# Performance work log

Hardware: AMD Instinct MI355X
Metric: run time of the kernel (lower is better)

Reference implementation:

```python
import jax, jax.numpy as jnp
import numpy as np

N_NODES = 100000
N_EDGES = 3200000
D_IN = 512
D_HID = 512
D_OUT = 256


def setup_inputs() -> dict:
    key = jax.random.key(0)
    ks = jax.random.split(key, 7)
    x = jax.random.normal(ks[0], (N_NODES, D_IN), dtype=jnp.float32)
    edge_row = jax.random.randint(ks[1], (N_EDGES,), 0, N_NODES, dtype=jnp.int32)
    edge_col = jax.random.randint(ks[2], (N_EDGES,), 0, N_NODES, dtype=jnp.int32)
    edge_val = jax.random.uniform(ks[3], (N_EDGES,), dtype=jnp.float32)
    # Kaiming-uniform-ish init like torch Linear (bias=False)
    W0 = jax.random.normal(ks[4], (D_HID, D_IN), dtype=jnp.float32) / np.sqrt(D_IN)
    W1 = jax.random.normal(ks[5], (D_HID, D_HID), dtype=jnp.float32) / np.sqrt(D_HID)
    W2 = jax.random.normal(ks[6], (D_OUT, D_HID), dtype=jnp.float32) / np.sqrt(D_HID)
    return {"x": x, "edge_row": edge_row, "edge_col": edge_col,
            "edge_val": edge_val, "W0": W0, "W1": W1, "W2": W2}


def reference(x, edge_row, edge_col, edge_val, W0, W1, W2):
    # Layer 0: Linear (no bias) then sparse adjacency matmul (COO segment-sum)
    h = jnp.einsum('nd,hd->nh', x, W0)                      # [N, D_HID]
    msgs = edge_val[:, None] * h[edge_col]                  # gather source features [E, D_HID]
    h = jax.ops.segment_sum(msgs, edge_row, num_segments=N_NODES)  # scatter-add to rows
    h = jax.nn.relu(h)                                      # dropout p=0.0 -> identity
    # Middle layer (num_hidden=3 -> one middle layer): Linear + ReLU
    h = jax.nn.relu(jnp.einsum('nd,hd->nh', h, W1))
    # Final layer: Linear only
    out = jnp.einsum('nd,od->no', h, W2)                    # [N, D_OUT]
    return out
```

## Files before the change

### kernel.cpp

```cpp
#include <hip/hip_runtime.h>

typedef short  s16x8 __attribute__((ext_vector_type(8)));
typedef __bf16 bf16x8 __attribute__((ext_vector_type(8)));
typedef float  f32x4 __attribute__((ext_vector_type(4)));

#define AS1(p) ((const __attribute__((address_space(1))) void*)(p))
#define AS3(p) ((__attribute__((address_space(3))) void*)(p))

__device__ __forceinline__ float bf2f(short x){
  unsigned u = ((unsigned)(unsigned short)x) << 16;
  return __builtin_bit_cast(float, u);
}

__global__ void cast_f32_bf16(const float* __restrict__ in, __bf16* __restrict__ out, int n8){
  int stride = gridDim.x * blockDim.x;
  for (int i = blockIdx.x * blockDim.x + threadIdx.x; i < n8; i += stride){
    const float4* p = (const float4*)in + 2*(size_t)i;
    float4 a = p[0], b = p[1];
    bf16x8 o;
    o[0]=(__bf16)a.x; o[1]=(__bf16)a.y; o[2]=(__bf16)a.z; o[3]=(__bf16)a.w;
    o[4]=(__bf16)b.x; o[5]=(__bf16)b.y; o[6]=(__bf16)b.z; o[7]=(__bf16)b.w;
    ((bf16x8*)out)[i] = o;
  }
}

__global__ void hist_rows(const int* __restrict__ rows, int* __restrict__ counts, int n){
  int stride = gridDim.x * blockDim.x;
  for (int i = blockIdx.x * blockDim.x + threadIdx.x; i < n; i += stride)
    atomicAdd(&counts[rows[i]], 1);
}

__global__ __launch_bounds__(256) void scan_phaseA(const int* __restrict__ counts,
    int* __restrict__ rp, int* __restrict__ bsum, int n4){
  __shared__ int sb[256];
  int t = threadIdx.x;
  int idx = blockIdx.x * 256 + t;
  int4 c = make_int4(0,0,0,0);
  if (idx < n4) c = ((const int4*)counts)[idx];
  int s = c.x + c.y + c.z + c.w;
  sb[t] = s; __syncthreads();
  #pragma unroll
  for (int d = 1; d < 256; d <<= 1){
    int v = (t >= d) ? sb[t - d] : 0;
    __syncthreads();
    sb[t] += v;
    __syncthreads();
  }
  int ex = sb[t] - s;
  if (idx < n4){
    int4 o; o.x = ex; o.y = ex + c.x; o.z = o.y + c.y; o.w = o.z + c.z;
    ((int4*)rp)[idx] = o;
  }
  if (t == 255) bsum[blockIdx.x] = sb[255];
}

__global__ __launch_bounds__(128) void scan_phaseB(int* __restrict__ bsum, int nb){
  __shared__ int sb[128];
  int t = threadIdx.x;
  int v = (t < nb) ? bsum[t] : 0;
  sb[t] = v; __syncthreads();
  #pragma unroll
  for (int d = 1; d < 128; d <<= 1){
    int u = (t >= d) ? sb[t - d] : 0;
    __syncthreads();
    sb[t] += u;
    __syncthreads();
  }
  if (t < nb) bsum[t] = sb[t] - v;
}

__global__ void scan_phaseC(const int* __restrict__ bsum, int* __restrict__ rp,
    int* __restrict__ cursor, int n, int ne){
  int i = blockIdx.x * 256 + threadIdx.x;
  if (i < n){
    int v = rp[i] + bsum[i >> 10];
    rp[i] = v; cursor[i] = v;
  }
  if (i == 0) rp[n] = ne;
}

__global__ void scatter_edges(const int* __restrict__ rows, const int* __restrict__ cols,
    const float* __restrict__ vals, int* __restrict__ cursor,
    int2* __restrict__ ev, int n){
  int stride = gridDim.x * blockDim.x;
  for (int i = blockIdx.x * blockDim.x + threadIdx.x; i < n; i += stride){
    int r = rows[i];
    int p = atomicAdd(&cursor[r], 1);
    ev[p] = make_int2(cols[i], __float_as_int(vals[i]));
  }
}

__global__ __launch_bounds__(256) void spmm_relu(
    const int* __restrict__ rp, const int2* __restrict__ ev,
    const __bf16* __restrict__ H, __bf16* __restrict__ O, int n){
  int w = (blockIdx.x * 256 + threadIdx.x) >> 6;
  int lane = threadIdx.x & 63;
  if (w >= n) return;
  int s = rp[w], e = rp[w + 1];
  int deg = e - s;
  const __bf16* Hl = H + lane * 8;
  float acc[8] = {0,0,0,0,0,0,0,0};

  int2 cv = make_int2(0, 0);
  if (lane < deg) cv = ev[s + lane];
  int m = deg < 64 ? deg : 64;
  int i = 0;
  for (; i + 4 <= m; i += 4){
    int c0 = __builtin_amdgcn_readlane(cv.x, i);
    int c1 = __builtin_amdgcn_readlane(cv.x, i + 1);
    int c2 = __builtin_amdgcn_readlane(cv.x, i + 2);
    int c3 = __builtin_amdgcn_readlane(cv.x, i + 3);
    float v0 = __builtin_bit_cast(float, __builtin_amdgcn_readlane(cv.y, i));
    float v1 = __builtin_bit_cast(float, __builtin_amdgcn_readlane(cv.y, i + 1));
    float v2 = __builtin_bit_cast(float, __builtin_amdgcn_readlane(cv.y, i + 2));
    float v3 = __builtin_bit_cast(float, __builtin_amdgcn_readlane(cv.y, i + 3));
    s16x8 h0 = *(const s16x8*)(Hl + (size_t)c0 * 512);
    s16x8 h1 = *(const s16x8*)(Hl + (size_t)c1 * 512);
    s16x8 h2 = *(const s16x8*)(Hl + (size_t)c2 * 512);
    s16x8 h3 = *(const s16x8*)(Hl + (size_t)c3 * 512);
    #pragma unroll
    for (int k = 0; k < 8; k++){
      acc[k] = fmaf(v0, bf2f(h0[k]), acc[k]);
      acc[k] = fmaf(v1, bf2f(h1[k]), acc[k]);
      acc[k] = fmaf(v2, bf2f(h2[k]), acc[k]);
      acc[k] = fmaf(v3, bf2f(h3[k]), acc[k]);
    }
  }
  for (; i < m; i++){
    int c = __builtin_amdgcn_readlane(cv.x, i);
    float v = __builtin_bit_cast(float, __builtin_amdgcn_readlane(cv.y, i));
    s16x8 h0 = *(const s16x8*)(Hl + (size_t)c * 512);
    #pragma unroll
    for (int k = 0; k < 8; k++) acc[k] = fmaf(v, bf2f(h0[k]), acc[k]);
  }
  for (int j = s + 64; j < e; j++){
    int2 p = ev[j];
    float v = __builtin_bit_cast(float, p.y);
    s16x8 h0 = *(const s16x8*)(Hl + (size_t)p.x * 512);
    #pragma unroll
    for (int k = 0; k < 8; k++) acc[k] = fmaf(v, bf2f(h0[k]), acc[k]);
  }

  s16x8 o;
  #pragma unroll
  for (int k = 0; k < 8; k++){
    float v = fmaxf(acc[k], 0.f);
    o[k] = __builtin_bit_cast(short, (__bf16)v);
  }
  *(s16x8*)(O + (size_t)w * 512 + lane * 8) = o;
}

template<int RELU, int OUT_BF16>
__global__ __launch_bounds__(256) void gemm_bt(
    const __bf16* __restrict__ A, const __bf16* __restrict__ B,
    void* __restrict__ C, int M, int N, int K){
  __shared__ __attribute__((aligned(16))) __bf16 As[128 * 64];
  __shared__ __attribute__((aligned(16))) __bf16 Bs[128 * 64];
  const int ntiles = N >> 7;
  const int tm = blockIdx.x / ntiles;
  const int tn = blockIdx.x % ntiles;
  const int row0 = tm << 7, col0 = tn << 7;
  const int tid = threadIdx.x;
  const int lane = tid & 63, wid = tid >> 6;
  const int wm = (wid >> 1) * 64, wn = (wid & 1) * 64;
  const int lr = lane & 15;
  const int lkb = ((lane >> 4) * 8) * 2;

  f32x4 acc[4][4] = {};

  for (int k0 = 0; k0 < K; k0 += 64){
    __syncthreads();
    #pragma unroll
    for (int i = 0; i < 4; i++){
      int bo = tid * 16 + i * 4096;
      int r  = bo >> 7;
      int cb = bo & 127;
      int ga = row0 + r; ga = ga < M ? ga : M - 1;
      __builtin_amdgcn_global_load_lds(AS1(A + (size_t)ga * K + k0 + (cb >> 1)),
                                       AS3((char*)As + (wid << 10) + i * 4096), 16, 0, 0);
      int gb = col0 + r;
      __builtin_amdgcn_global_load_lds(AS1(B + (size_t)gb * K + k0 + (cb >> 1)),
                                       AS3((char*)Bs + (wid << 10) + i * 4096), 16, 0, 0);
    }
    __syncthreads();
    #pragma unroll
    for (int kk = 0; kk < 2; kk++){
      s16x8 af[4], bfr[4];
      #pragma unroll
      for (int i = 0; i < 4; i++)
        af[i] = *(const s16x8*)((const char*)As + (wm + i * 16 + lr) * 128 + kk * 64 + lkb);
      #pragma unroll
      for (int j = 0; j < 4; j++)
        bfr[j] = *(const s16x8*)((const char*)Bs + (wn + j * 16 + lr) * 128 + kk * 64 + lkb);
      #pragma unroll
      for (int i = 0; i < 4; i++)
        #pragma unroll
        for (int j = 0; j < 4; j++)
          acc[i][j] = __builtin_amdgcn_mfma_f32_16x16x32_bf16(af[i], bfr[j], acc[i][j], 0, 0, 0);
    }
  }

  const int orow = (lane >> 4) * 4;
  #pragma unroll
  for (int i = 0; i < 4; i++){
    #pragma unroll
    for (int j = 0; j < 4; j++){
      int gc = col0 + wn + j * 16 + lr;
      #pragma unroll
      for (int r = 0; r < 4; r++){
        int gr = row0 + wm + i * 16 + orow + r;
        if (gr < M){
          float v = acc[i][j][r];
          if (RELU) v = fmaxf(v, 0.f);
          if (OUT_BF16) ((__bf16*)C)[(size_t)gr * N + gc] = (__bf16)v;
          else          ((float*)C)[(size_t)gr * N + gc] = v;
        }
      }
    }
  }
}

extern "C" void kernel_launch(void* const* d_in, const int* in_sizes, int n_in,
                              void* d_out, int out_size, void* d_ws, size_t ws_size,
                              hipStream_t stream){
  const float* x    = (const float*)d_in[0];
  const int*   erow = (const int*)d_in[1];
  const int*   ecol = (const int*)d_in[2];
  const float* eval = (const float*)d_in[3];
  const float* W0   = (const float*)d_in[4];
  const float* W1   = (const float*)d_in[5];
  const float* W2   = (const float*)d_in[6];

  const int DIN = 512, DH = 512, DO = 256;
  const int NN = in_sizes[0] / DIN;
  const int NE = in_sizes[1];

  size_t off = 0;
  auto carve = [&](size_t b) -> char* {
    char* p = (char*)d_ws + off; off += (b + 255) & ~(size_t)255; return p;
  };
  __bf16* bufA  = (__bf16*)carve((size_t)NN * DIN * 2);
  __bf16* bufB  = (__bf16*)carve((size_t)NN * DH * 2);
  __bf16* wW0   = (__bf16*)carve((size_t)DH * DIN * 2);
  __bf16* wW1   = (__bf16*)carve((size_t)DH * DH * 2);
  __bf16* wW2   = (__bf16*)carve((size_t)DO * DH * 2);
  int*   counts = (int*)carve((size_t)NN * 4);
  int*   rp     = (int*)carve(((size_t)NN + 1) * 4);
  int*   cursor = (int*)carve((size_t)NN * 4);
  int*   bsum   = (int*)carve(4096);
  int2*  ev     = (int2*)carve((size_t)NE * 8);

  hipMemsetAsync(counts, 0, (size_t)NN * 4, stream);

  cast_f32_bf16<<<4096, 256, 0, stream>>>(x,  bufA, NN * DIN / 8);
  cast_f32_bf16<<<256,  256, 0, stream>>>(W0, wW0, DH * DIN / 8);
  cast_f32_bf16<<<256,  256, 0, stream>>>(W1, wW1, DH * DH / 8);
  cast_f32_bf16<<<128,  256, 0, stream>>>(W2, wW2, DO * DH / 8);

  hist_rows<<<2048, 256, 0, stream>>>(erow, counts, NE);
  const int n4 = NN / 4;
  const int nblkA = (n4 + 255) / 256;
  scan_phaseA<<<nblkA, 256, 0, stream>>>(counts, rp, bsum, n4);
  scan_phaseB<<<1, 128, 0, stream>>>(bsum, nblkA);
  scan_phaseC<<<(NN + 255) / 256, 256, 0, stream>>>(bsum, rp, cursor, NN, NE);
  scatter_edges<<<2048, 256, 0, stream>>>(erow, ecol, eval, cursor, ev, NE);

  const int mt = (NN + 127) / 128;
  gemm_bt<0,1><<<dim3(mt * (DH / 128)), 256, 0, stream>>>(bufA, wW0, bufB, NN, DH, DIN);
  spmm_relu<<<(NN * 64 + 255) / 256, 256, 0, stream>>>(rp, ev, bufB, bufA, NN);
  gemm_bt<1,1><<<dim3(mt * (DH / 128)), 256, 0, stream>>>(bufA, wW1, bufB, NN, DH, DH);
  gemm_bt<0,0><<<dim3(mt * (DO / 128)), 256, 0, stream>>>(bufB, wW2, d_out, NN, DO, DH);
}
```

Measured before the change: 1.450 ms.

## Persistent SpMM waves with next-row prefetch, XCD-aware GEMM tile remap, fuse weight casts

The SpMM kernel becomes persistent: 2048 blocks' waves loop over rows with a stride and prefetch the next row's pointers and edge list while the current row is being computed. This hides the latency of the row-pointer and edge loads and cuts wave launch overhead. The GEMM remaps block indices so consecutive tiles land on the same XCD, which should improve L2 reuse of the A row panels. The three weight cast launches are merged into one kernel to save launch overhead. The risk is that the fixed grid may load-balance poorly across rows of different degree.

```diff
diff --git a/kernel.cpp b/kernel.cpp
--- a/kernel.cpp
+++ b/kernel.cpp
@@ -21,6 +21,25 @@
     o[0]=(__bf16)a.x; o[1]=(__bf16)a.y; o[2]=(__bf16)a.z; o[3]=(__bf16)a.w;
     o[4]=(__bf16)b.x; o[5]=(__bf16)b.y; o[6]=(__bf16)b.z; o[7]=(__bf16)b.w;
     ((bf16x8*)out)[i] = o;
+  }
+}
+
+__global__ void cast3_f32_bf16(const float* __restrict__ a, __bf16* __restrict__ oa, int na8,
+                               const float* __restrict__ b, __bf16* __restrict__ ob, int nb8,
+                               const float* __restrict__ c, __bf16* __restrict__ oc, int nc8){
+  int stride = gridDim.x * blockDim.x;
+  int tot = na8 + nb8 + nc8;
+  for (int i = blockIdx.x * blockDim.x + threadIdx.x; i < tot; i += stride){
+    const float* in; __bf16* out; int j = i;
+    if (j < na8){ in = a; out = oa; }
+    else if (j < na8 + nb8){ j -= na8; in = b; out = ob; }
+    else { j -= na8 + nb8; in = c; out = oc; }
+    const float4* p = (const float4*)in + 2*(size_t)j;
+    float4 u = p[0], v = p[1];
+    bf16x8 o;
+    o[0]=(__bf16)u.x; o[1]=(__bf16)u.y; o[2]=(__bf16)u.z; o[3]=(__bf16)u.w;
+    o[4]=(__bf16)v.x; o[5]=(__bf16)v.y; o[6]=(__bf16)v.z; o[7]=(__bf16)v.w;
+    ((bf16x8*)out)[j] = o;
   }
 }
 
@@ -92,62 +111,76 @@
 
 __global__ __launch_bounds__(256) void spmm_relu(
     const int* __restrict__ rp, const int2* __restrict__ ev,
-    const __bf16* __restrict__ H, __bf16* __restrict__ O, int n){
+    const __bf16* __restrict__ H, __bf16* __restrict__ O, int n, int nwaves){
+  int lane = threadIdx.x & 63;
   int w = (blockIdx.x * 256 + threadIdx.x) >> 6;
-  int lane = threadIdx.x & 63;
   if (w >= n) return;
+  const __bf16* Hl = H + lane * 8;
+
   int s = rp[w], e = rp[w + 1];
-  int deg = e - s;
-  const __bf16* Hl = H + lane * 8;
-  float acc[8] = {0,0,0,0,0,0,0,0};
-
   int2 cv = make_int2(0, 0);
-  if (lane < deg) cv = ev[s + lane];
-  int m = deg < 64 ? deg : 64;
-  int i = 0;
-  for (; i + 4 <= m; i += 4){
-    int c0 = __builtin_amdgcn_readlane(cv.x, i);
-    int c1 = __builtin_amdgcn_readlane(cv.x, i + 1);
-    int c2 = __builtin_amdgcn_readlane(cv.x, i + 2);
-    int c3 = __builtin_amdgcn_readlane(cv.x, i + 3);
-    float v0 = __builtin_bit_cast(float, __builtin_amdgcn_readlane(cv.y, i));
-    float v1 = __builtin_bit_cast(float, __builtin_amdgcn_readlane(cv.y, i + 1));
-    float v2 = __builtin_bit_cast(float, __builtin_amdgcn_readlane(cv.y, i + 2));
-    float v3 = __builtin_bit_cast(float, __builtin_amdgcn_readlane(cv.y, i + 3));
-    s16x8 h0 = *(const s16x8*)(Hl + (size_t)c0 * 512);
-    s16x8 h1 = *(const s16x8*)(Hl + (size_t)c1 * 512);
-    s16x8 h2 = *(const s16x8*)(Hl + (size_t)c2 * 512);
-    s16x8 h3 = *(const s16x8*)(Hl + (size_t)c3 * 512);
+  if (lane < e - s) cv = ev[s + lane];
+
+  while (true){
+    int wn = w + nwaves;
+    int sn = 0, en = 0;
+    int2 cvn = make_int2(0, 0);
+    if (wn < n){
+      sn = rp[wn]; en = rp[wn + 1];
+      if (lane < en - sn) cvn = ev[sn + lane];
+    }
+
+    float acc[8] = {0,0,0,0,0,0,0,0};
+    int deg = e - s;
+    int m = deg < 64 ? deg : 64;
+    int i = 0;
+    for (; i + 4 <= m; i += 4){
+      int c0 = __builtin_amdgcn_readlane(cv.x, i);
+      int c1 = __builtin_amdgcn_readlane(cv.x, i + 1);
+      int c2 = __builtin_amdgcn_readlane(cv.x, i + 2);
+      int c3 = __builtin_amdgcn_readlane(cv.x, i + 3);
+      float v0 = __builtin_bit_cast(float, __builtin_amdgcn_readlane(cv.y, i));
+      float v1 = __builtin_bit_cast(float, __builtin_amdgcn_readlane(cv.y, i + 1));
+      float v2 = __builtin_bit_cast(float, __builtin_amdgcn_readlane(cv.y, i + 2));
+      float v3 = __builtin_bit_cast(float, __builtin_amdgcn_readlane(cv.y, i + 3));
+      s16x8 h0 = *(const s16x8*)(Hl + (size_t)c0 * 512);
+      s16x8 h1 = *(const s16x8*)(Hl + (size_t)c1 * 512);
+      s16x8 h2 = *(const s16x8*)(Hl + (size_t)c2 * 512);
+      s16x8 h3 = *(const s16x8*)(Hl + (size_t)c3 * 512);
+      #pragma unroll
+      for (int k = 0; k < 8; k++){
+        acc[k] = fmaf(v0, bf2f(h0[k]), acc[k]);
+        acc[k] = fmaf(v1, bf2f(h1[k]), acc[k]);
+        acc[k] = fmaf(v2, bf2f(h2[k]), acc[k]);
+        acc[k] = fmaf(v3, bf2f(h3[k]), acc[k]);
+      }
+    }
+    for (; i < m; i++){
+      int c = __builtin_amdgcn_readlane(cv.x, i);
+      float v = __builtin_bit_cast(float, __builtin_amdgcn_readlane(cv.y, i));
+      s16x8 h0 = *(const s16x8*)(Hl + (size_t)c * 512);
+      #pragma unroll
+      for (int k = 0; k < 8; k++) acc[k] = fmaf(v, bf2f(h0[k]), acc[k]);
+    }
+    for (int j = s + 64; j < e; j++){
+      int2 p = ev[j];
+      float v = __builtin_bit_cast(float, p.y);
+      s16x8 h0 = *(const s16x8*)(Hl + (size_t)p.x * 512);
+      #pragma unroll
+      for (int k = 0; k < 8; k++) acc[k] = fmaf(v, bf2f(h0[k]), acc[k]);
+    }
+
+    s16x8 o;
     #pragma unroll
     for (int k = 0; k < 8; k++){
-      acc[k] = fmaf(v0, bf2f(h0[k]), acc[k]);
-      acc[k] = fmaf(v1, bf2f(h1[k]), acc[k]);
-      acc[k] = fmaf(v2, bf2f(h2[k]), acc[k]);
-      acc[k] = fmaf(v3, bf2f(h3[k]), acc[k]);
-    }
-  }
-  for (; i < m; i++){
-    int c = __builtin_amdgcn_readlane(cv.x, i);
-    float v = __builtin_bit_cast(float, __builtin_amdgcn_readlane(cv.y, i));
-    s16x8 h0 = *(const s16x8*)(Hl + (size_t)c * 512);
-    #pragma unroll
-    for (int k = 0; k < 8; k++) acc[k] = fmaf(v, bf2f(h0[k]), acc[k]);
-  }
-  for (int j = s + 64; j < e; j++){
-    int2 p = ev[j];
-    float v = __builtin_bit_cast(float, p.y);
-    s16x8 h0 = *(const s16x8*)(Hl + (size_t)p.x * 512);
-    #pragma unroll
-    for (int k = 0; k < 8; k++) acc[k] = fmaf(v, bf2f(h0[k]), acc[k]);
-  }
-
-  s16x8 o;
-  #pragma unroll
-  for (int k = 0; k < 8; k++){
-    float v = fmaxf(acc[k], 0.f);
-    o[k] = __builtin_bit_cast(short, (__bf16)v);
-  }
-  *(s16x8*)(O + (size_t)w * 512 + lane * 8) = o;
+      float v = fmaxf(acc[k], 0.f);
+      o[k] = __builtin_bit_cast(short, (__bf16)v);
+    }
+    *(s16x8*)(O + (size_t)w * 512 + lane * 8) = o;
+
+    if (wn >= n) break;
+    w = wn; s = sn; e = en; cv = cvn;
+  }
 }
 
 template<int RELU, int OUT_BF16>
@@ -156,9 +189,13 @@
     void* __restrict__ C, int M, int N, int K){
   __shared__ __attribute__((aligned(16))) __bf16 As[128 * 64];
   __shared__ __attribute__((aligned(16))) __bf16 Bs[128 * 64];
+  const int nwg = gridDim.x;
+  const int q = nwg >> 3, r = nwg & 7;
+  const int xcd = blockIdx.x & 7, idx = blockIdx.x >> 3;
+  const int wg = (xcd < r ? xcd * (q + 1) : r * (q + 1) + (xcd - r) * q) + idx;
   const int ntiles = N >> 7;
-  const int tm = blockIdx.x / ntiles;
-  const int tn = blockIdx.x % ntiles;
+  const int tm = wg / ntiles;
+  const int tn = wg % ntiles;
   const int row0 = tm << 7, col0 = tn << 7;
   const int tid = threadIdx.x;
   const int lane = tid & 63, wid = tid >> 6;
@@ -173,12 +210,12 @@
     #pragma unroll
     for (int i = 0; i < 4; i++){
       int bo = tid * 16 + i * 4096;
-      int r  = bo >> 7;
+      int rr = bo >> 7;
       int cb = bo & 127;
-      int ga = row0 + r; ga = ga < M ? ga : M - 1;
+      int ga = row0 + rr; ga = ga < M ? ga : M - 1;
       __builtin_amdgcn_global_load_lds(AS1(A + (size_t)ga * K + k0 + (cb >> 1)),
                                        AS3((char*)As + (wid << 10) + i * 4096), 16, 0, 0);
-      int gb = col0 + r;
+      int gb = col0 + rr;
       __builtin_amdgcn_global_load_lds(AS1(B + (size_t)gb * K + k0 + (cb >> 1)),
                                        AS3((char*)Bs + (wid << 10) + i * 4096), 16, 0, 0);
     }
@@ -207,10 +244,10 @@
     for (int j = 0; j < 4; j++){
       int gc = col0 + wn + j * 16 + lr;
       #pragma unroll
-      for (int r = 0; r < 4; r++){
-        int gr = row0 + wm + i * 16 + orow + r;
+      for (int rr = 0; rr < 4; rr++){
+        int gr = row0 + wm + i * 16 + orow + rr;
         if (gr < M){
-          float v = acc[i][j][r];
+          float v = acc[i][j][rr];
           if (RELU) v = fmaxf(v, 0.f);
           if (OUT_BF16) ((__bf16*)C)[(size_t)gr * N + gc] = (__bf16)v;
           else          ((float*)C)[(size_t)gr * N + gc] = v;
@@ -252,10 +289,10 @@
 
   hipMemsetAsync(counts, 0, (size_t)NN * 4, stream);
 
-  cast_f32_bf16<<<4096, 256, 0, stream>>>(x,  bufA, NN * DIN / 8);
-  cast_f32_bf16<<<256,  256, 0, stream>>>(W0, wW0, DH * DIN / 8);
-  cast_f32_bf16<<<256,  256, 0, stream>>>(W1, wW1, DH * DH / 8);
-  cast_f32_bf16<<<128,  256, 0, stream>>>(W2, wW2, DO * DH / 8);
+  cast_f32_bf16<<<4096, 256, 0, stream>>>(x, bufA, NN * DIN / 8);
+  cast3_f32_bf16<<<512, 256, 0, stream>>>(W0, wW0, DH * DIN / 8,
+                                          W1, wW1, DH * DH / 8,
+                                          W2, wW2, DO * DH / 8);
 
   hist_rows<<<2048, 256, 0, stream>>>(erow, counts, NE);
   const int n4 = NN / 4;
@@ -267,7 +304,8 @@
 
   const int mt = (NN + 127) / 128;
   gemm_bt<0,1><<<dim3(mt * (DH / 128)), 256, 0, stream>>>(bufA, wW0, bufB, NN, DH, DIN);
-  spmm_relu<<<(NN * 64 + 255) / 256, 256, 0, stream>>>(rp, ev, bufB, bufA, NN);
+  const int nwv = 2048 * 4;
+  spmm_relu<<<2048, 256, 0, stream>>>(rp, ev, bufB, bufA, NN, nwv);
   gemm_bt<1,1><<<dim3(mt * (DH / 128)), 256, 0, stream>>>(bufA, wW1, bufB, NN, DH, DH);
   gemm_bt<0,0><<<dim3(mt * (DO / 128)), 256, 0, stream>>>(bufB, wW2, d_out, NN, DO, DH);
 }
```

New measurement: 1.464 ms. About the same (+1.0%).
